# Kernel optimization log

Hardware: AMD Instinct MI355X
Metric: run time of the kernel (lower is better)

## Reference

```python
import jax, jax.numpy as jnp
import numpy as np

ALPHA = 0.05   # propalpha
GDEP = 2       # gcn_depth
DIL = 2        # new_dilation
KSET = (2, 3, 6, 7)

def _dconv(x, w, b, d):
    # Conv2d(c_in, c_out, (1, k), dilation=(1, d), padding='same'), NCHW layout
    k = w.shape[-1]
    tot = d * (k - 1)
    lo = tot // 2
    y = jax.lax.conv_general_dilated(x, w, (1, 1), ((0, 0), (lo, tot - lo)),
                                     rhs_dilation=(1, d),
                                     dimension_numbers=('NCHW', 'OIHW', 'NCHW'))
    return y + b[None, :, None, None]

def _inception(x, ws, bs):
    # 'same' padding keeps seq_len for every branch, so the tail-slice is a no-op
    return jnp.concatenate([_dconv(x, w, b, DIL) for w, b in zip(ws, bs)], axis=1)

def _gcn(Hf, Aoff, W, b, n):
    # PyG GCNConv with unit edge weights (no edge_weight passed) and remaining self-loops:
    # out = D^-1/2 (A_off + I_R)^T D^-1/2 (Hf @ W^T) + b, where only rows < n carry edges.
    XW = Hf @ W.T
    deg = jnp.ones((Hf.shape[0],), Hf.dtype).at[:n].add(jnp.sum(Aoff, axis=0))
    dis = jax.lax.rsqrt(deg)
    out = XW / deg[:, None]                                           # self-loop term
    out = out.at[:n].add(dis[:n, None] * (Aoff.T @ (dis[:n, None] * XW[:n])))
    return out + b[None, :]

def _mixprop(X, A, gws, gbs, mw, mb):
    B, C, n, L = X.shape
    # dense_to_sparse ignores weights here (none passed to GCNConv) -> binary adjacency;
    # add_remaining_self_loops replaces any diagonal entries, so zero the diagonal.
    Aoff = (A != 0).astype(X.dtype) * (1.0 - jnp.eye(n, dtype=X.dtype))
    H = X
    hops = [X]
    for i in range(GDEP):
        Hf = H.reshape(B * L, C * n)   # torch row-major reshape, replicated exactly
        H1 = _gcn(Hf, Aoff, gws[i], gbs[i], n)
        H = ALPHA * X + H1.reshape(B, C, n, L)
        hops.append(H)
    Hc = jnp.concatenate(hops, axis=1)  # (B, (GDEP+1)*C, n, L)
    return jnp.einsum('bixl,oi->boxl', Hc, mw) + mb[None, :, None, None]

def _layernorm(x, w, b, idx, eps=1e-5):
    # F.layer_norm over all of x.shape[1:] with node-indexed affine params
    mu = jnp.mean(x, axis=(1, 2, 3), keepdims=True)
    var = jnp.var(x, axis=(1, 2, 3), keepdims=True)
    xh = (x - mu) * jax.lax.rsqrt(var + eps)
    return xh * w[:, idx, :][None] + b[:, idx, :][None]

def _forward(x, x_skip, A, idx, fws, fbs, gws, gbs, skip_w, skip_b,
             mp1_gw, mp1_gb, mp1_mw, mp1_mb, mp2_gw, mp2_gb, mp2_mw, mp2_mb,
             ln_w, ln_b):
    x_res = x
    xf = jnp.tanh(_inception(x, fws, fbs))
    xg = jax.nn.sigmoid(_inception(x, gws, gbs))
    x = xf * xg  # gated dilated temporal conv (dropout is an eval-mode no-op)
    x_skip = jnp.einsum('bixl,oi->boxl', x, skip_w) + skip_b[None, :, None, None] + x_skip
    x = (_mixprop(x, A, mp1_gw, mp1_gb, mp1_mw, mp1_mb)
         + _mixprop(x.swapaxes(0, 0), A.T, mp2_gw, mp2_gb, mp2_mw, mp2_mb))
    x = x + x_res[..., -x.shape[3]:]
    x = _layernorm(x, ln_w, ln_b, idx)
    return x, x_skip

def setup_inputs():
    key = jax.random.key(0)
    ks = jax.random.split(key, 32)
    B, C, N, L, SKIP = 16, 32, 128, 128, 64
    F = C * N
    co = C // len(KSET)
    d = {}
    d['x'] = jax.random.normal(ks[0], (B, C, N, L), jnp.float32)
    d['x_skip'] = jax.random.normal(ks[1], (B, SKIP, N, L), jnp.float32)
    d['A'] = jax.random.uniform(ks[2], (N, N), jnp.float32)
    d['idx'] = jnp.arange(N, dtype=jnp.int32)
    i = 3
    for pre in ('f', 'g'):
        for k in KSET:
            d[pre + 'w' + str(k)] = jax.random.normal(ks[i], (co, C, 1, k), jnp.float32) * float(1.0 / np.sqrt(C * k))
            d[pre + 'b' + str(k)] = jax.random.uniform(ks[i + 1], (co,), jnp.float32)
            i += 2
    d['skip_w'] = jax.random.normal(ks[i], (SKIP, C), jnp.float32) * float(1.0 / np.sqrt(C)); i += 1
    d['skip_b'] = jax.random.uniform(ks[i], (SKIP,), jnp.float32); i += 1
    for mp in ('mp1', 'mp2'):
        d[mp + '_gw'] = jax.random.normal(ks[i], (GDEP, F, F), jnp.float32) * float(1.0 / np.sqrt(F)); i += 1
        d[mp + '_gb'] = jnp.zeros((GDEP, F), jnp.float32)
        d[mp + '_mw'] = jax.random.normal(ks[i], (C, (GDEP + 1) * C), jnp.float32) * float(1.0 / np.sqrt((GDEP + 1) * C)); i += 1
        d[mp + '_mb'] = jax.random.uniform(ks[i], (C,), jnp.float32); i += 1
    d['ln_w'] = jnp.ones((C, N, L), jnp.float32)
    d['ln_b'] = jnp.zeros((C, N, L), jnp.float32)
    return d

def reference(x, x_skip, A, idx, fw2, fb2, fw3, fb3, fw6, fb6, fw7, fb7,
              gw2, gb2, gw3, gb3, gw6, gb6, gw7, gb7, skip_w, skip_b,
              mp1_gw, mp1_gb, mp1_mw, mp1_mb, mp2_gw, mp2_gb, mp2_mw, mp2_mb,
              ln_w, ln_b):
    return _forward(x, x_skip, A, idx,
                    [fw2, fw3, fw6, fw7], [fb2, fb3, fb6, fb7],
                    [gw2, gw3, gw6, gw7], [gb2, gb3, gb6, gb7],
                    skip_w, skip_b, mp1_gw, mp1_gb, mp1_mw, mp1_mb,
                    mp2_gw, mp2_gb, mp2_mw, mp2_mb, ln_w, ln_b)
```

## Files before the change

kernel.cpp:

```cpp
#include <hip/hip_runtime.h>
#include <stdint.h>

typedef unsigned short u16;
typedef unsigned int   u32;
typedef __attribute__((ext_vector_type(4))) float f32x4;
typedef __attribute__((ext_vector_type(8))) short bf16x8;

__device__ __forceinline__ u16 f2bf(float f) {
    u32 i = __float_as_uint(f);
    u32 r = (i + 0x7fffu + ((i >> 16) & 1u)) >> 16;
    return (u16)r;
}
__device__ __forceinline__ float bf2f(u16 u) {
    return __uint_as_float(((u32)u) << 16);
}
__device__ __forceinline__ u32 cvt2bf(float a, float b) {
    u32 r;
    asm("v_cvt_pk_bf16_f32 %0, %1, %2" : "=v"(r) : "v"(a), "v"(b));
    return r;
}

#define GLOAD16(g, l) __builtin_amdgcn_global_load_lds( \
    (const __attribute__((address_space(1))) void*)(g), \
    (__attribute__((address_space(3))) void*)(l), 16, 0, 0)

#define RAW_BARRIER()  asm volatile("s_barrier" ::: "memory")
#define VMCNT(n)       asm volatile("s_waitcnt vmcnt(" #n ")" ::: "memory")

__global__ void k_prep(const float* __restrict__ A, float* dis1, float* inv1,
                       float* dis2, float* inv2)
{
    int r = threadIdx.x;
    if (r >= 128) return;
    int cc = 0, cr = 0;
    for (int j = 0; j < 128; ++j) {
        if (j == r) continue;
        if (A[(j << 7) + r] != 0.f) cc++;
        if (A[(r << 7) + j] != 0.f) cr++;
    }
    float d1 = 1.f + (float)cc, d2 = 1.f + (float)cr;
    dis1[r] = rsqrtf(d1); inv1[r] = 1.f / d1;
    dis2[r] = rsqrtf(d2); inv2[r] = 1.f / d2;
}

__global__ __launch_bounds__(256)
void k_wcvt2(const float* __restrict__ W0, const float* __restrict__ W1,
             u16* __restrict__ Wb0, u16* __restrict__ Wb1)
{
    int half = blockIdx.x >> 13;
    const float* W = half ? W1 : W0;
    u16* Wb = half ? Wb1 : Wb0;
    size_t e = ((size_t)(blockIdx.x & 8191) * 256 + threadIdx.x) * 8;
    f32x4 a = *(const f32x4*)(W + e);
    f32x4 b = *(const f32x4*)(W + e + 4);
    uint4 r;
    r.x = cvt2bf(a[0], a[1]); r.y = cvt2bf(a[2], a[3]);
    r.z = cvt2bf(b[0], b[1]); r.w = cvt2bf(b[2], b[3]);
    *(uint4*)(Wb + e) = r;
}

__global__ __launch_bounds__(512, 1)
void k_gemm2g(const u16* __restrict__ A0, const u16* __restrict__ A1,
              const u16* __restrict__ B0, const u16* __restrict__ B1,
              const u16* __restrict__ Gres,
              const float* __restrict__ gb0, const float* __restrict__ gb1,
              u16* __restrict__ Ha, u16* __restrict__ Hb,
              float* __restrict__ XW0a, float* __restrict__ XW0b)
{
    __shared__ alignas(16) u16 LDS[65536];
    const int NT = 128;
    const int tid  = threadIdx.x;
    const int lane = tid & 63;
    const int wid  = tid >> 6;
    const int wr = wid >> 2, wc = wid & 3;

    const int bid = blockIdx.x;
    const int swz = (bid & 7) * 32 + (bid >> 3);
    const int z   = swz >> 7;
    const int rem = swz & 127;
    const int bm = (rem >> 4) * 256;
    const int bn = (rem & 15) * 256;

    const u16* Ap = (z ? A1 : A0) + (size_t)bm * 4096;
    const u16* Bp = (z ? B1 : B0) + (size_t)bn * 4096;

    int aoff[8], boff[4];
    #pragma unroll
    for (int i = 0; i < 8; ++i) {
        int row = wr * 128 + i * 16 + (lane & 15);
        int sp  = (lane >> 4) ^ ((row >> 1) & 3);
        aoff[i] = row * 32 + sp * 8;
    }
    #pragma unroll
    for (int j = 0; j < 4; ++j) {
        int row = wc * 64 + j * 16 + (lane & 15);
        int sp  = (lane >> 4) ^ ((row >> 1) & 3);
        boff[j] = row * 32 + sp * 8;
    }

    auto stage = [&](int t) {
        if (t >= NT) return;
        const int k0  = t << 5;
        u16* buf = LDS + ((t & 3) << 14);
        #pragma unroll
        for (int h = 0; h < 2; ++h) {
            const int c  = tid + h * 512;
            const int r  = c >> 2;
            const int sl = (c & 3) ^ ((r >> 1) & 3);
            GLOAD16(Ap + (size_t)r * 4096 + k0 + sl * 8, buf + c * 8);
            GLOAD16(Bp + (size_t)r * 4096 + k0 + sl * 8, buf + 8192 + c * 8);
        }
    };

    f32x4 acc[8][4] = {};

    auto compute = [&](int t) {
        const u16* buf = LDS + ((t & 3) << 14);
        bf16x8 af[8], bf[4];
        #pragma unroll
        for (int j = 0; j < 4; ++j) bf[j] = *(const bf16x8*)(buf + 8192 + boff[j]);
        #pragma unroll
        for (int i = 0; i < 8; ++i) af[i] = *(const bf16x8*)(buf + aoff[i]);
        __builtin_amdgcn_s_setprio(1);
        #pragma unroll
        for (int i = 0; i < 8; ++i)
            #pragma unroll
            for (int j = 0; j < 4; ++j)
                acc[i][j] = __builtin_amdgcn_mfma_f32_16x16x32_bf16(af[i], bf[j], acc[i][j], 0, 0, 0);
        __builtin_amdgcn_s_setprio(0);
    };

    stage(0); stage(1); stage(2);
    for (int t = 0; t < NT - 3; ++t) {
        VMCNT(8);
        RAW_BARRIER();
        stage(t + 3);
        compute(t);
    }
    VMCNT(8);  RAW_BARRIER(); compute(NT - 3);
    VMCNT(4);  RAW_BARRIER(); compute(NT - 2);
    VMCNT(0);  RAW_BARRIER(); compute(NT - 1);

    const int orow = (lane >> 4) * 4, ocol = lane & 15;
    const float* gbv = z ? gb1 : gb0;
    u16* H = z ? Hb : Ha;

    #pragma unroll
    for (int j = 0; j < 4; ++j) {
        const int o = bn + wc * 64 + j * 16 + ocol;
        const float gbo = gbv[o];
        #pragma unroll
        for (int i = 0; i < 8; ++i) {
            const int rbase = bm + wr * 128 + i * 16 + orow;
            #pragma unroll
            for (int v = 0; v < 4; ++v) {
                const size_t e = (size_t)(rbase + v) * 4096 + o;
                float g = bf2f(Gres[e]);
                H[e] = f2bf(__fmaf_rn(0.05f, g, acc[i][j][v] + gbo));
            }
        }
    }
    if (bm == 0 && wr == 0) {
        float* XW0 = z ? XW0b : XW0a;
        #pragma unroll
        for (int i = 0; i < 8; ++i) {
            #pragma unroll
            for (int j = 0; j < 4; ++j) {
                float* cp = XW0 + (size_t)(i * 16 + orow) * 4096 + (bn + wc * 64 + j * 16 + ocol);
                #pragma unroll
                for (int v = 0; v < 4; ++v)
                    cp[(size_t)v * 4096] = acc[i][j][v];
            }
        }
    }
}

__global__ __launch_bounds__(256)
void k_gcnfix(const float* __restrict__ XW0a, const float* __restrict__ XW0b,
              const u16* __restrict__ G, const float* __restrict__ Af,
              const float* __restrict__ dis1, const float* __restrict__ inv1,
              const float* __restrict__ dis2, const float* __restrict__ inv2,
              const float* __restrict__ gb0, const float* __restrict__ gb1,
              u16* __restrict__ Ha, u16* __restrict__ Hb)
{
    const int prob = blockIdx.x >> 9;
    const int rem  = blockIdx.x & 511;
    const int t4 = rem * 256 + threadIdx.x;
    const int r = t4 >> 10, og = (t4 & 1023) << 2;
    const float* XW0 = prob ? XW0b : XW0a;
    const float* dis = prob ? dis2 : dis1;
    const float* inv = prob ? inv2 : inv1;
    const float* gb  = prob ? gb1  : gb0;
    u16* H = prob ? Hb : Ha;

    const size_t e = ((size_t)r << 12) + og;
    f32x4 xw = *(const f32x4*)(XW0 + e);
    f32x4 s = {0.f, 0.f, 0.f, 0.f};
    for (int j = 0; j < 128; ++j) {
        float av = prob ? Af[(r << 7) + j] : Af[(j << 7) + r];
        float wv = ((av != 0.f) && (j != r)) ? dis[j] : 0.f;
        f32x4 xv = *(const f32x4*)(XW0 + ((size_t)j << 12) + og);
        #pragma unroll
        for (int q = 0; q < 4; ++q) s[q] = __fmaf_rn(wv, xv[q], s[q]);
    }
    const float iv = inv[r], dr = dis[r];
    f32x4 gb4 = *(const f32x4*)(gb + og);
    uint2 gv = *(const uint2*)(G + e);
    float g0 = __uint_as_float(gv.x << 16), g1 = __uint_as_float(gv.x & 0xffff0000u);
    float g2 = __uint_as_float(gv.y << 16), g3 = __uint_as_float(gv.y & 0xffff0000u);
    float y0 = __fmaf_rn(0.05f, g0, __fmaf_rn(dr, s[0], xw[0] * iv) + gb4[0]);
    float y1 = __fmaf_rn(0.05f, g1, __fmaf_rn(dr, s[1], xw[1] * iv) + gb4[1]);
    float y2 = __fmaf_rn(0.05f, g2, __fmaf_rn(dr, s[2], xw[2] * iv) + gb4[2]);
    float y3 = __fmaf_rn(0.05f, g3, __fmaf_rn(dr, s[3], xw[3] * iv) + gb4[3]);
    uint2 rr;
    rr.x = cvt2bf(y0, y1);
    rr.y = cvt2bf(y2, y3);
    *(uint2*)(H + e) = rr;
}

__device__ __forceinline__ constexpr int wbase_of(int k) {
    return k == 2 ? 0 : k == 3 ? 520 : k == 6 ? 1296 : 2840;
}
__device__ __forceinline__ constexpr int ob_of(int k) {
    return k == 2 ? 0 : k == 3 ? 8 : k == 6 ? 16 : 24;
}

template<int K_>
__device__ __forceinline__ void conv_phase(const float* __restrict__ xsb,
                                           const float* __restrict__ wfp,
                                           const float* __restrict__ wgp,
                                           float fb, float gb,
                                           u16* __restrict__ Gp)
{
    float accf[8], accg[8];
    #pragma unroll
    for (int i = 0; i < 8; ++i) { accf[i] = fb; accg[i] = gb; }
    for (int c = 0; c < 32; ++c) {
        float xw[24];
        const float* xr = xsb + c * 144;
        #pragma unroll
        for (int q = 0; q < 6; ++q) {
            f32x4 v = *(const f32x4*)(xr + q * 4);
            xw[q * 4 + 0] = v[0]; xw[q * 4 + 1] = v[1];
            xw[q * 4 + 2] = v[2]; xw[q * 4 + 3] = v[3];
        }
        float wfj[K_], wgj[K_];
        const float* wfc = wfp + c * K_;
        const float* wgc = wgp + c * K_;
        #pragma unroll
        for (int j = 0; j < K_; ++j) { wfj[j] = wfc[j]; wgj[j] = wgc[j]; }
        #pragma unroll
        for (int li = 0; li < 8; ++li) {
            #pragma unroll
            for (int j = 0; j < K_; ++j) {
                float xv = xw[li + 8 - (K_ - 1) + 2 * j];
                accf[li] = __fmaf_rn(xv, wfj[j], accf[li]);
                accg[li] = __fmaf_rn(xv, wgj[j], accg[li]);
            }
        }
    }
    u16 o8[8];
    #pragma unroll
    for (int i = 0; i < 8; ++i) {
        float e2 = __expf(2.f * accf[i]);
        float th = 1.f - __fdividef(2.f, e2 + 1.f);
        float sg = __fdividef(1.f, 1.f + __expf(-accg[i]));
        o8[i] = f2bf(th * sg);
    }
    uint4 u;
    u.x = o8[0] | ((u32)o8[1] << 16); u.y = o8[2] | ((u32)o8[3] << 16);
    u.z = o8[4] | ((u32)o8[5] << 16); u.w = o8[6] | ((u32)o8[7] << 16);
    *(uint4*)Gp = u;
}

template<int KA, int KB>
__device__ __forceinline__ void wave_pair(const float* __restrict__ xs,
                                          const float* __restrict__ wfl,
                                          const float* __restrict__ wgl,
                                          const float* __restrict__ fbl,
                                          const float* __restrict__ gbl,
                                          int oo, int lL, int b, int n,
                                          u16* __restrict__ G)
{
    {
        constexpr int BS = wbase_of(KA), ST = 32 * KA + 1, OB = ob_of(KA);
        const int o = OB + oo, l0 = lL * 8;
        conv_phase<KA>(xs + l0, wfl + BS + oo * ST, wgl + BS + oo * ST,
                       fbl[o], gbl[o],
                       G + (((size_t)(b * 32 + o) * 128 + n) * 128 + l0));
    }
    {
        constexpr int BS = wbase_of(KB), ST = 32 * KB + 1, OB = ob_of(KB);
        const int o = OB + oo, l0 = 64 + lL * 8;
        conv_phase<KB>(xs + l0, wfl + BS + oo * ST, wgl + BS + oo * ST,
                       fbl[o], gbl[o],
                       G + (((size_t)(b * 32 + o) * 128 + n) * 128 + l0));
    }
}

__global__ __launch_bounds__(256)
void k_incep(const float* __restrict__ x,
             const float* __restrict__ fw2p, const float* __restrict__ fw3p,
             const float* __restrict__ fw6p, const float* __restrict__ fw7p,
             const float* __restrict__ fb2p, const float* __restrict__ fb3p,
             const float* __restrict__ fb6p, const float* __restrict__ fb7p,
             const float* __restrict__ gw2p, const float* __restrict__ gw3p,
             const float* __restrict__ gw6p, const float* __restrict__ gw7p,
             const float* __restrict__ gb2p, const float* __restrict__ gb3p,
             const float* __restrict__ gb6p, const float* __restrict__ gb7p,
             u16* __restrict__ G)
{
    __shared__ alignas(16) float xs[32 * 144];
    __shared__ float wfl[4640], wgl[4640];
    __shared__ float fbl[32], gbl[32];
    const int tid = threadIdx.x;
    const int b = blockIdx.x >> 7, n = blockIdx.x & 127;

    for (int i = tid; i < 32 * 144; i += 256) xs[i] = 0.f;
    for (int g = tid; g < 4608; g += 256) {
        int rel, k, woff;
        const float *pf, *pg;
        if (g < 512)       { rel = g;        k = 2; woff = 0;    pf = fw2p; pg = gw2p; }
        else if (g < 1280) { rel = g - 512;  k = 3; woff = 520;  pf = fw3p; pg = gw3p; }
        else if (g < 2816) { rel = g - 1280; k = 6; woff = 1296; pf = fw6p; pg = gw6p; }
        else               { rel = g - 2816; k = 7; woff = 2840; pf = fw7p; pg = gw7p; }
        int ck = 32 * k;
        int oo = rel / ck, rem = rel % ck;
        int dst = woff + oo * (ck + 1) + rem;
        wfl[dst] = pf[rel];
        wgl[dst] = pg[rel];
    }
    if (tid < 32) {
        int br = tid >> 3, oo = tid & 7;
        const float* pf = br == 0 ? fb2p : br == 1 ? fb3p : br == 2 ? fb6p : fb7p;
        const float* pg = br == 0 ? gb2p : br == 1 ? gb3p : br == 2 ? gb6p : gb7p;
        fbl[tid] = pf[oo]; gbl[tid] = pg[oo];
    }
    __syncthreads();
    const float* xb = x + (size_t)b * 524288 + n * 128;
    for (int p = 0; p < 4; ++p) {
        int chunk = p * 256 + tid;
        int c = chunk >> 5, l4 = (chunk & 31) * 4;
        *(f32x4*)&xs[c * 144 + 8 + l4] = *(const f32x4*)(xb + (size_t)c * 16384 + l4);
    }
    __syncthreads();

    const int w = tid >> 6, lane = tid & 63;
    const int oo = lane >> 3, lL = lane & 7;
    switch (w) {
        case 0:  wave_pair<2, 7>(xs, wfl, wgl, fbl, gbl, oo, lL, b, n, G); break;
        case 1:  wave_pair<7, 2>(xs, wfl, wgl, fbl, gbl, oo, lL, b, n, G); break;
        case 2:  wave_pair<3, 6>(xs, wfl, wgl, fbl, gbl, oo, lL, b, n, G); break;
        default: wave_pair<6, 3>(xs, wfl, wgl, fbl, gbl, oo, lL, b, n, G); break;
    }
}

__global__ __launch_bounds__(256)
void k_skip(const u16* __restrict__ G, const float* __restrict__ xskip,
            const float* __restrict__ sw, const float* __restrict__ sb,
            float* __restrict__ outp)
{
    __shared__ alignas(16) u16 Gs[4096];
    __shared__ float swl[64 * 33];
    __shared__ float sbl[64];
    const int tid = threadIdx.x;
    const int b = blockIdx.x >> 7, n = blockIdx.x & 127;
    const u16* gb_ = G + (size_t)b * 524288 + n * 128;
    for (int p = 0; p < 2; ++p) {
        int chunk = p * 256 + tid, c = chunk >> 4, l8 = (chunk & 15) * 8;
        *(uint4*)&Gs[c * 128 + l8] = *(const uint4*)(gb_ + (size_t)c * 16384 + l8);
    }
    for (int i = tid; i < 2048; i += 256) swl[(i >> 5) * 33 + (i & 31)] = sw[i];
    if (tid < 64) sbl[tid] = sb[tid];
    __syncthreads();
    const int sg = (tid & 15) * 4, l0 = (tid >> 4) * 8;
    float acc[4][8];
    #pragma unroll
    for (int si = 0; si < 4; ++si) {
        float bv = sbl[sg + si];
        #pragma unroll
        for (int li = 0; li < 8; ++li) acc[si][li] = bv;
    }
    for (int c = 0; c < 32; ++c) {
        uint4 gv = *(const uint4*)&Gs[c * 128 + l0];
        float g[8];
        g[0] = __uint_as_float(gv.x << 16); g[1] = __uint_as_float(gv.x & 0xffff0000u);
        g[2] = __uint_as_float(gv.y << 16); g[3] = __uint_as_float(gv.y & 0xffff0000u);
        g[4] = __uint_as_float(gv.z << 16); g[5] = __uint_as_float(gv.z & 0xffff0000u);
        g[6] = __uint_as_float(gv.w << 16); g[7] = __uint_as_float(gv.w & 0xffff0000u);
        #pragma unroll
        for (int si = 0; si < 4; ++si) {
            float wv = swl[(sg + si) * 33 + c];
            #pragma unroll
            for (int li = 0; li < 8; ++li) acc[si][li] = __fmaf_rn(g[li], wv, acc[si][li]);
        }
    }
    #pragma unroll
    for (int si = 0; si < 4; ++si) {
        size_t e = ((size_t)(b * 64 + sg + si) * 128 + n) * 128 + l0;
        f32x4 x0 = *(const f32x4*)(xskip + e);
        f32x4 x1 = *(const f32x4*)(xskip + e + 4);
        f32x4 r0, r1;
        r0[0] = acc[si][0] + x0[0]; r0[1] = acc[si][1] + x0[1];
        r0[2] = acc[si][2] + x0[2]; r0[3] = acc[si][3] + x0[3];
        r1[0] = acc[si][4] + x1[0]; r1[1] = acc[si][5] + x1[1];
        r1[2] = acc[si][6] + x1[2]; r1[3] = acc[si][7] + x1[3];
        *(f32x4*)(outp + e)     = r0;
        *(f32x4*)(outp + e + 4) = r1;
    }
}

__global__ __launch_bounds__(256)
void k_mix2ln(const u16* __restrict__ G,
              const u16* __restrict__ H1, const u16* __restrict__ H2,
              const u16* __restrict__ H1b, const u16* __restrict__ H2b,
              const float* __restrict__ mw1, const float* __restrict__ mb1,
              const float* __restrict__ mw2, const float* __restrict__ mb2,
              const float* __restrict__ x,
              u16* __restrict__ Y, float* __restrict__ partial)
{
    __shared__ alignas(16) u16 Gs[4096], H1s[4096], H2s[4096], H1bs[4096], H2bs[4096];
    __shared__ float wSg[32 * 33], wS11[32 * 33], wS12[32 * 33], wS21[32 * 33], wS22[32 * 33];
    __shared__ float mbl[32];
    const int tid = threadIdx.x;
    const int b = blockIdx.x >> 7, xn = blockIdx.x & 127;
    size_t base = (size_t)b * 524288 + xn * 128;
    for (int p = 0; p < 2; ++p) {
        int chunk = p * 256 + tid, c = chunk >> 4, l8 = (chunk & 15) * 8;
        size_t src = base + (size_t)c * 16384 + l8;
        *(uint4*)&Gs[c * 128 + l8]   = *(const uint4*)(G + src);
        *(uint4*)&H1s[c * 128 + l8]  = *(const uint4*)(H1 + src);
        *(uint4*)&H2s[c * 128 + l8]  = *(const uint4*)(H2 + src);
        *(uint4*)&H1bs[c * 128 + l8] = *(const uint4*)(H1b + src);
        *(uint4*)&H2bs[c * 128 + l8] = *(const uint4*)(H2b + src);
    }
    for (int i = tid; i < 1024; i += 256) {
        int o = i >> 5, c = i & 31;
        int d = o * 33 + c;
        wSg[d]  = mw1[o * 96 + c] + mw2[o * 96 + c];
        wS11[d] = mw1[o * 96 + 32 + c];
        wS12[d] = mw1[o * 96 + 64 + c];
        wS21[d] = mw2[o * 96 + 32 + c];
        wS22[d] = mw2[o * 96 + 64 + c];
    }
    if (tid < 32) mbl[tid] = mb1[tid] + mb2[tid];
    __syncthreads();
    const int og = (tid & 7) * 4, l0 = (tid >> 3) * 4;
    float acc[4][4];
    #pragma unroll
    for (int oi = 0; oi < 4; ++oi) {
        float bv = mbl[og + oi];
        acc[oi][0] = bv; acc[oi][1] = bv; acc[oi][2] = bv; acc[oi][3] = bv;
    }
    for (int c = 0; c < 32; ++c) {
        uint2 ga = *(const uint2*)&Gs[c * 128 + l0];
        uint2 h1 = *(const uint2*)&H1s[c * 128 + l0];
        uint2 h2 = *(const uint2*)&H2s[c * 128 + l0];
        uint2 j1 = *(const uint2*)&H1bs[c * 128 + l0];
        uint2 j2 = *(const uint2*)&H2bs[c * 128 + l0];
        float gv[4], v1[4], v2[4], u1[4], u2[4];
        gv[0] = __uint_as_float(ga.x << 16); gv[1] = __uint_as_float(ga.x & 0xffff0000u);
        gv[2] = __uint_as_float(ga.y << 16); gv[3] = __uint_as_float(ga.y & 0xffff0000u);
        v1[0] = __uint_as_float(h1.x << 16); v1[1] = __uint_as_float(h1.x & 0xffff0000u);
        v1[2] = __uint_as_float(h1.y << 16); v1[3] = __uint_as_float(h1.y & 0xffff0000u);
        v2[0] = __uint_as_float(h2.x << 16); v2[1] = __uint_as_float(h2.x & 0xffff0000u);
        v2[2] = __uint_as_float(h2.y << 16); v2[3] = __uint_as_float(h2.y & 0xffff0000u);
        u1[0] = __uint_as_float(j1.x << 16); u1[1] = __uint_as_float(j1.x & 0xffff0000u);
        u1[2] = __uint_as_float(j1.y << 16); u1[3] = __uint_as_float(j1.y & 0xffff0000u);
        u2[0] = __uint_as_float(j2.x << 16); u2[1] = __uint_as_float(j2.x & 0xffff0000u);
        u2[2] = __uint_as_float(j2.y << 16); u2[3] = __uint_as_float(j2.y & 0xffff0000u);
        #pragma unroll
        for (int oi = 0; oi < 4; ++oi) {
            int d = (og + oi) * 33 + c;
            float a0 = wSg[d], a1 = wS11[d], a2 = wS12[d], a3 = wS21[d], a4 = wS22[d];
            #pragma unroll
            for (int li = 0; li < 4; ++li)
                acc[oi][li] += gv[li] * a0 + v1[li] * a1 + v2[li] * a2
                             + u1[li] * a3 + u2[li] * a4;
        }
    }
    float s = 0.f, ss = 0.f;
    #pragma unroll
    for (int oi = 0; oi < 4; ++oi) {
        size_t e = ((size_t)(b * 32 + og + oi) * 128 + xn) * 128 + l0;
        f32x4 xv = *(const f32x4*)(x + e);
        float y0 = acc[oi][0] + xv[0];
        float y1 = acc[oi][1] + xv[1];
        float y2 = acc[oi][2] + xv[2];
        float y3 = acc[oi][3] + xv[3];
        s  += y0 + y1 + y2 + y3;
        ss += y0 * y0 + y1 * y1 + y2 * y2 + y3 * y3;
        uint2 rr;
        rr.x = cvt2bf(y0, y1);
        rr.y = cvt2bf(y2, y3);
        *(uint2*)(Y + e) = rr;
    }
    #pragma unroll
    for (int o = 32; o > 0; o >>= 1) {
        s  += __shfl_down(s,  o, 64);
        ss += __shfl_down(ss, o, 64);
    }
    __shared__ float sred[8];
    int w = tid >> 6;
    if ((tid & 63) == 0) { sred[w * 2] = s; sred[w * 2 + 1] = ss; }
    __syncthreads();
    if (tid == 0) {
        partial[blockIdx.x * 2]     = sred[0] + sred[2] + sred[4] + sred[6];
        partial[blockIdx.x * 2 + 1] = sred[1] + sred[3] + sred[5] + sred[7];
    }
}

__global__ __launch_bounds__(256)
void k_lnnorm(const u16* __restrict__ Y,
              const float* __restrict__ partial, const int* __restrict__ idxp,
              const float* __restrict__ lnw, const float* __restrict__ lnb,
              float* __restrict__ outx)
{
    const int tid = threadIdx.x;
    const int b = blockIdx.x >> 7, chunk = blockIdx.x & 127;
    float s = 0.f, ss = 0.f;
    if (tid < 128) {
        s  = partial[(b * 128 + tid) * 2];
        ss = partial[(b * 128 + tid) * 2 + 1];
    }
    #pragma unroll
    for (int o = 32; o > 0; o >>= 1) {
        s  += __shfl_down(s,  o, 64);
        ss += __shfl_down(ss, o, 64);
    }
    __shared__ float sred[4];
    __shared__ float mv[2];
    if ((tid & 63) == 0 && tid < 128) { sred[(tid >> 6) * 2] = s; sred[(tid >> 6) * 2 + 1] = ss; }
    __syncthreads();
    if (tid == 0) {
        float S = sred[0] + sred[2], SS = sred[1] + sred[3];
        float mean = S * (1.f / 524288.f);
        float var = SS * (1.f / 524288.f) - mean * mean;
        mv[0] = mean; mv[1] = rsqrtf(var + 1e-5f);
    }
    __syncthreads();
    const float mean = mv[0], rstd = mv[1];
    #pragma unroll
    for (int q = 0; q < 4; ++q) {
        int ib = chunk * 4096 + q * 1024 + tid * 4;
        size_t e = (size_t)b * 524288 + ib;
        uint2 yv2 = *(const uint2*)(Y + e);
        float y[4];
        y[0] = __uint_as_float(yv2.x << 16); y[1] = __uint_as_float(yv2.x & 0xffff0000u);
        y[2] = __uint_as_float(yv2.y << 16); y[3] = __uint_as_float(yv2.y & 0xffff0000u);
        int c = ib >> 14, xn = (ib >> 7) & 127, l = ib & 127;
        int ix = idxp[xn];
        size_t we = ((size_t)c * 128 + ix) * 128 + l;
        f32x4 wv = *(const f32x4*)(lnw + we);
        f32x4 bv = *(const f32x4*)(lnb + we);
        f32x4 r;
        #pragma unroll
        for (int j = 0; j < 4; ++j)
            r[j] = (y[j] - mean) * rstd * wv[j] + bv[j];
        *(f32x4*)(outx + e) = r;
    }
}

extern "C" void kernel_launch(void* const* d_in, const int* in_sizes, int n_in,
                              void* d_out, int out_size, void* d_ws, size_t ws_size,
                              hipStream_t stream)
{
    (void)in_sizes; (void)n_in; (void)out_size; (void)ws_size;
    const float* x      = (const float*)d_in[0];
    const float* xskip  = (const float*)d_in[1];
    const float* A      = (const float*)d_in[2];
    const int*   idxp   = (const int*)d_in[3];
    const float* fw2p = (const float*)d_in[4];  const float* fb2p = (const float*)d_in[5];
    const float* fw3p = (const float*)d_in[6];  const float* fb3p = (const float*)d_in[7];
    const float* fw6p = (const float*)d_in[8];  const float* fb6p = (const float*)d_in[9];
    const float* fw7p = (const float*)d_in[10]; const float* fb7p = (const float*)d_in[11];
    const float* gw2p = (const float*)d_in[12]; const float* gb2p = (const float*)d_in[13];
    const float* gw3p = (const float*)d_in[14]; const float* gb3p = (const float*)d_in[15];
    const float* gw6p = (const float*)d_in[16]; const float* gb6p = (const float*)d_in[17];
    const float* gw7p = (const float*)d_in[18]; const float* gb7p = (const float*)d_in[19];
    const float* sw   = (const float*)d_in[20]; const float* sb   = (const float*)d_in[21];
    const float* mp1_gw = (const float*)d_in[22]; const float* mp1_gb = (const float*)d_in[23];
    const float* mp1_mw = (const float*)d_in[24]; const float* mp1_mb = (const float*)d_in[25];
    const float* mp2_gw = (const float*)d_in[26]; const float* mp2_gb = (const float*)d_in[27];
    const float* mp2_mw = (const float*)d_in[28]; const float* mp2_mb = (const float*)d_in[29];
    const float* lnw = (const float*)d_in[30]; const float* lnb = (const float*)d_in[31];

    char* wsb = (char*)d_ws;
    float* out_x  = (float*)d_out;
    float* out_sk = out_x + 8388608;

    const size_t MB16 = 16777216, MB33 = 33554432;
    u16*   G    = (u16*)(wsb);
    u16*   H1   = (u16*)(wsb + MB16);
    u16*   H1b  = (u16*)(wsb + 2 * MB16);
    u16*   H2   = (u16*)(wsb + 3 * MB16);
    u16*   H2b  = (u16*)(wsb + 4 * MB16);
    u16*   Wb0  = (u16*)(wsb + 5 * MB16);
    u16*   Wb1  = (u16*)(wsb + 5 * MB16 + MB33);
    u16*   Yb   = (u16*)Wb0;
    float* XW0a = (float*)(wsb + 5 * MB16 + 2 * MB33);
    float* XW0b = (float*)(wsb + 5 * MB16 + 2 * MB33 + 2097152);
    float* part = (float*)(wsb + 5 * MB16 + 2 * MB33 + 4194304);
    float* dd   = (float*)(wsb + 5 * MB16 + 2 * MB33 + 4194304 + 16384);
    float *dis1 = dd, *inv1 = dd + 128, *dis2 = dd + 256, *inv2 = dd + 384;

    k_prep<<<1, 128, 0, stream>>>(A, dis1, inv1, dis2, inv2);
    k_incep<<<2048, 256, 0, stream>>>(x, fw2p, fw3p, fw6p, fw7p, fb2p, fb3p, fb6p, fb7p,
                                      gw2p, gw3p, gw6p, gw7p, gb2p, gb3p, gb6p, gb7p, G);
    k_skip<<<2048, 256, 0, stream>>>(G, xskip, sw, sb, out_sk);

    k_wcvt2<<<16384, 256, 0, stream>>>(mp1_gw, mp2_gw, Wb0, Wb1);
    k_gemm2g<<<256, 512, 0, stream>>>(G, G, Wb0, Wb1, G, mp1_gb, mp2_gb,
                                      H1, H1b, XW0a, XW0b);
    k_gcnfix<<<1024, 256, 0, stream>>>(XW0a, XW0b, G, A, dis1, inv1, dis2, inv2,
                                       mp1_gb, mp2_gb, H1, H1b);
    k_wcvt2<<<16384, 256, 0, stream>>>(mp1_gw + MB16, mp2_gw + MB16, Wb0, Wb1);
    k_gemm2g<<<256, 512, 0, stream>>>(H1, H1b, Wb0, Wb1, G, mp1_gb + 4096, mp2_gb + 4096,
                                      H2, H2b, XW0a, XW0b);
    k_gcnfix<<<1024, 256, 0, stream>>>(XW0a, XW0b, G, A, dis1, inv1, dis2, inv2,
                                       mp1_gb + 4096, mp2_gb + 4096, H2, H2b);
    k_mix2ln<<<2048, 256, 0, stream>>>(G, H1, H2, H1b, H2b, mp1_mw, mp1_mb,
                                       mp2_mw, mp2_mb, x, Yb, part);
    k_lnnorm<<<2048, 256, 0, stream>>>(Yb, part, idxp, lnw, lnb, out_x);
}
```

Baseline: 669.4 us.

## Fuse inception conv and skip conv into one kernel sharing LDS tile

Merges the inception kernel and the skip-conv kernel so the gated conv output is written both to global memory and to shared memory, and the skip 1x1 conv then reads it from LDS instead of re-reading G from global. This removes one kernel launch and a global read of G. The per-wave work is also reorganised: each wave now computes two branches at once over the same input window with interleaved accumulators, where before it handled two branches one after the other on different halves of the sequence. This adds LDS usage and register pressure, which may lower occupancy.

```diff
diff --git a/kernel.cpp b/kernel.cpp
--- a/kernel.cpp
+++ b/kernel.cpp
@@ -225,16 +225,22 @@
     return k == 2 ? 0 : k == 3 ? 8 : k == 6 ? 16 : 24;
 }
 
-template<int K_>
-__device__ __forceinline__ void conv_phase(const float* __restrict__ xsb,
-                                           const float* __restrict__ wfp,
-                                           const float* __restrict__ wgp,
-                                           float fb, float gb,
-                                           u16* __restrict__ Gp)
-{
-    float accf[8], accg[8];
-    #pragma unroll
-    for (int i = 0; i < 8; ++i) { accf[i] = fb; accg[i] = gb; }
+template<int KA, int KB>
+__device__ __forceinline__ void conv_dual(const float* __restrict__ xsb,
+                                          const float* __restrict__ wfA,
+                                          const float* __restrict__ wgA,
+                                          const float* __restrict__ wfB,
+                                          const float* __restrict__ wgB,
+                                          float fbA, float gbA, float fbB, float gbB,
+                                          u16* __restrict__ GpA, u16* __restrict__ GpB,
+                                          u16* __restrict__ GsA, u16* __restrict__ GsB)
+{
+    float afA[8], agA[8], afB[8], agB[8];
+    #pragma unroll
+    for (int i = 0; i < 8; ++i) {
+        afA[i] = fbA; agA[i] = gbA;
+        afB[i] = fbB; agB[i] = gbB;
+    }
     for (int c = 0; c < 32; ++c) {
         float xw[24];
         const float* xr = xsb + c * 144;
@@ -244,75 +250,80 @@
             xw[q * 4 + 0] = v[0]; xw[q * 4 + 1] = v[1];
             xw[q * 4 + 2] = v[2]; xw[q * 4 + 3] = v[3];
         }
-        float wfj[K_], wgj[K_];
-        const float* wfc = wfp + c * K_;
-        const float* wgc = wgp + c * K_;
-        #pragma unroll
-        for (int j = 0; j < K_; ++j) { wfj[j] = wfc[j]; wgj[j] = wgc[j]; }
-        #pragma unroll
-        for (int li = 0; li < 8; ++li) {
-            #pragma unroll
-            for (int j = 0; j < K_; ++j) {
-                float xv = xw[li + 8 - (K_ - 1) + 2 * j];
-                accf[li] = __fmaf_rn(xv, wfj[j], accf[li]);
-                accg[li] = __fmaf_rn(xv, wgj[j], accg[li]);
+        {
+            float wf[KA], wg[KA];
+            const float* pf = wfA + c * KA;
+            const float* pg = wgA + c * KA;
+            #pragma unroll
+            for (int j = 0; j < KA; ++j) { wf[j] = pf[j]; wg[j] = pg[j]; }
+            #pragma unroll
+            for (int li = 0; li < 8; ++li) {
+                #pragma unroll
+                for (int j = 0; j < KA; ++j) {
+                    float xv = xw[li + 8 - (KA - 1) + 2 * j];
+                    afA[li] = __fmaf_rn(xv, wf[j], afA[li]);
+                    agA[li] = __fmaf_rn(xv, wg[j], agA[li]);
+                }
             }
         }
-    }
-    u16 o8[8];
+        {
+            float wf[KB], wg[KB];
+            const float* pf = wfB + c * KB;
+            const float* pg = wgB + c * KB;
+            #pragma unroll
+            for (int j = 0; j < KB; ++j) { wf[j] = pf[j]; wg[j] = pg[j]; }
+            #pragma unroll
+            for (int li = 0; li < 8; ++li) {
+                #pragma unroll
+                for (int j = 0; j < KB; ++j) {
+                    float xv = xw[li + 8 - (KB - 1) + 2 * j];
+                    afB[li] = __fmaf_rn(xv, wf[j], afB[li]);
+                    agB[li] = __fmaf_rn(xv, wg[j], agB[li]);
+                }
+            }
+        }
+    }
+    u16 oA[8], oB[8];
     #pragma unroll
     for (int i = 0; i < 8; ++i) {
-        float e2 = __expf(2.f * accf[i]);
+        float e2 = __expf(2.f * afA[i]);
         float th = 1.f - __fdividef(2.f, e2 + 1.f);
-        float sg = __fdividef(1.f, 1.f + __expf(-accg[i]));
-        o8[i] = f2bf(th * sg);
-    }
-    uint4 u;
-    u.x = o8[0] | ((u32)o8[1] << 16); u.y = o8[2] | ((u32)o8[3] << 16);
-    u.z = o8[4] | ((u32)o8[5] << 16); u.w = o8[6] | ((u32)o8[7] << 16);
-    *(uint4*)Gp = u;
-}
-
-template<int KA, int KB>
-__device__ __forceinline__ void wave_pair(const float* __restrict__ xs,
-                                          const float* __restrict__ wfl,
-                                          const float* __restrict__ wgl,
-                                          const float* __restrict__ fbl,
-                                          const float* __restrict__ gbl,
-                                          int oo, int lL, int b, int n,
-                                          u16* __restrict__ G)
-{
-    {
-        constexpr int BS = wbase_of(KA), ST = 32 * KA + 1, OB = ob_of(KA);
-        const int o = OB + oo, l0 = lL * 8;
-        conv_phase<KA>(xs + l0, wfl + BS + oo * ST, wgl + BS + oo * ST,
-                       fbl[o], gbl[o],
-                       G + (((size_t)(b * 32 + o) * 128 + n) * 128 + l0));
-    }
-    {
-        constexpr int BS = wbase_of(KB), ST = 32 * KB + 1, OB = ob_of(KB);
-        const int o = OB + oo, l0 = 64 + lL * 8;
-        conv_phase<KB>(xs + l0, wfl + BS + oo * ST, wgl + BS + oo * ST,
-                       fbl[o], gbl[o],
-                       G + (((size_t)(b * 32 + o) * 128 + n) * 128 + l0));
-    }
+        float sg = __fdividef(1.f, 1.f + __expf(-agA[i]));
+        oA[i] = f2bf(th * sg);
+        float e2b = __expf(2.f * afB[i]);
+        float thb = 1.f - __fdividef(2.f, e2b + 1.f);
+        float sgb = __fdividef(1.f, 1.f + __expf(-agB[i]));
+        oB[i] = f2bf(thb * sgb);
+    }
+    uint4 uA, uB;
+    uA.x = oA[0] | ((u32)oA[1] << 16); uA.y = oA[2] | ((u32)oA[3] << 16);
+    uA.z = oA[4] | ((u32)oA[5] << 16); uA.w = oA[6] | ((u32)oA[7] << 16);
+    uB.x = oB[0] | ((u32)oB[1] << 16); uB.y = oB[2] | ((u32)oB[3] << 16);
+    uB.z = oB[4] | ((u32)oB[5] << 16); uB.w = oB[6] | ((u32)oB[7] << 16);
+    *(uint4*)GpA = uA; *(uint4*)GpB = uB;
+    *(uint4*)GsA = uA; *(uint4*)GsB = uB;
 }
 
 __global__ __launch_bounds__(256)
-void k_incep(const float* __restrict__ x,
-             const float* __restrict__ fw2p, const float* __restrict__ fw3p,
-             const float* __restrict__ fw6p, const float* __restrict__ fw7p,
-             const float* __restrict__ fb2p, const float* __restrict__ fb3p,
-             const float* __restrict__ fb6p, const float* __restrict__ fb7p,
-             const float* __restrict__ gw2p, const float* __restrict__ gw3p,
-             const float* __restrict__ gw6p, const float* __restrict__ gw7p,
-             const float* __restrict__ gb2p, const float* __restrict__ gb3p,
-             const float* __restrict__ gb6p, const float* __restrict__ gb7p,
-             u16* __restrict__ G)
+void k_incskip(const float* __restrict__ x,
+               const float* __restrict__ fw2p, const float* __restrict__ fw3p,
+               const float* __restrict__ fw6p, const float* __restrict__ fw7p,
+               const float* __restrict__ fb2p, const float* __restrict__ fb3p,
+               const float* __restrict__ fb6p, const float* __restrict__ fb7p,
+               const float* __restrict__ gw2p, const float* __restrict__ gw3p,
+               const float* __restrict__ gw6p, const float* __restrict__ gw7p,
+               const float* __restrict__ gb2p, const float* __restrict__ gb3p,
+               const float* __restrict__ gb6p, const float* __restrict__ gb7p,
+               const float* __restrict__ sw,   const float* __restrict__ sb,
+               const float* __restrict__ xskip,
+               u16* __restrict__ G, float* __restrict__ outp)
 {
     __shared__ alignas(16) float xs[32 * 144];
     __shared__ float wfl[4640], wgl[4640];
     __shared__ float fbl[32], gbl[32];
+    __shared__ alignas(16) u16 Gs[4096];
+    __shared__ float swl[64 * 33];
+    __shared__ float sbl[64];
     const int tid = threadIdx.x;
     const int b = blockIdx.x >> 7, n = blockIdx.x & 127;
 
@@ -330,6 +341,8 @@
         wfl[dst] = pf[rel];
         wgl[dst] = pg[rel];
     }
+    for (int i = tid; i < 2048; i += 256) swl[(i >> 5) * 33 + (i & 31)] = sw[i];
+    if (tid < 64) sbl[tid] = sb[tid];
     if (tid < 32) {
         int br = tid >> 3, oo = tid & 7;
         const float* pf = br == 0 ? fb2p : br == 1 ? fb3p : br == 2 ? fb6p : fb7p;
@@ -345,35 +358,36 @@
     }
     __syncthreads();
 
-    const int w = tid >> 6, lane = tid & 63;
-    const int oo = lane >> 3, lL = lane & 7;
-    switch (w) {
-        case 0:  wave_pair<2, 7>(xs, wfl, wgl, fbl, gbl, oo, lL, b, n, G); break;
-        case 1:  wave_pair<7, 2>(xs, wfl, wgl, fbl, gbl, oo, lL, b, n, G); break;
-        case 2:  wave_pair<3, 6>(xs, wfl, wgl, fbl, gbl, oo, lL, b, n, G); break;
-        default: wave_pair<6, 3>(xs, wfl, wgl, fbl, gbl, oo, lL, b, n, G); break;
-    }
-}
-
-__global__ __launch_bounds__(256)
-void k_skip(const u16* __restrict__ G, const float* __restrict__ xskip,
-            const float* __restrict__ sw, const float* __restrict__ sb,
-            float* __restrict__ outp)
-{
-    __shared__ alignas(16) u16 Gs[4096];
-    __shared__ float swl[64 * 33];
-    __shared__ float sbl[64];
-    const int tid = threadIdx.x;
-    const int b = blockIdx.x >> 7, n = blockIdx.x & 127;
-    const u16* gb_ = G + (size_t)b * 524288 + n * 128;
-    for (int p = 0; p < 2; ++p) {
-        int chunk = p * 256 + tid, c = chunk >> 4, l8 = (chunk & 15) * 8;
-        *(uint4*)&Gs[c * 128 + l8] = *(const uint4*)(gb_ + (size_t)c * 16384 + l8);
-    }
-    for (int i = tid; i < 2048; i += 256) swl[(i >> 5) * 33 + (i & 31)] = sw[i];
-    if (tid < 64) sbl[tid] = sb[tid];
+    {
+        const int w = tid >> 6, lane = tid & 63;
+        const int oo = lane >> 3, lL = lane & 7;
+        const int h  = w & 1;
+        const int l0 = h * 64 + lL * 8;
+        const float* xsb = xs + l0;
+        size_t gbase = ((size_t)b * 32 * 128 + n) * 128 + l0;
+        if (w < 2) {
+            constexpr int KA = 2, KB = 7;
+            const int oA = ob_of(KA) + oo, oB = ob_of(KB) + oo;
+            conv_dual<KA, KB>(xsb,
+                wfl + wbase_of(KA) + oo * (32 * KA + 1), wgl + wbase_of(KA) + oo * (32 * KA + 1),
+                wfl + wbase_of(KB) + oo * (32 * KB + 1), wgl + wbase_of(KB) + oo * (32 * KB + 1),
+                fbl[oA], gbl[oA], fbl[oB], gbl[oB],
+                G + gbase + (size_t)oA * 16384, G + gbase + (size_t)oB * 16384,
+                Gs + oA * 128 + l0, Gs + oB * 128 + l0);
+        } else {
+            constexpr int KA = 3, KB = 6;
+            const int oA = ob_of(KA) + oo, oB = ob_of(KB) + oo;
+            conv_dual<KA, KB>(xsb,
+                wfl + wbase_of(KA) + oo * (32 * KA + 1), wgl + wbase_of(KA) + oo * (32 * KA + 1),
+                wfl + wbase_of(KB) + oo * (32 * KB + 1), wgl + wbase_of(KB) + oo * (32 * KB + 1),
+                fbl[oA], gbl[oA], fbl[oB], gbl[oB],
+                G + gbase + (size_t)oA * 16384, G + gbase + (size_t)oB * 16384,
+                Gs + oA * 128 + l0, Gs + oB * 128 + l0);
+        }
+    }
     __syncthreads();
-    const int sg = (tid & 15) * 4, l0 = (tid >> 4) * 8;
+
+    const int sg = (tid & 15) * 4, l0s = (tid >> 4) * 8;
     float acc[4][8];
     #pragma unroll
     for (int si = 0; si < 4; ++si) {
@@ -382,7 +396,7 @@
         for (int li = 0; li < 8; ++li) acc[si][li] = bv;
     }
     for (int c = 0; c < 32; ++c) {
-        uint4 gv = *(const uint4*)&Gs[c * 128 + l0];
+        uint4 gv = *(const uint4*)&Gs[c * 128 + l0s];
         float g[8];
         g[0] = __uint_as_float(gv.x << 16); g[1] = __uint_as_float(gv.x & 0xffff0000u);
         g[2] = __uint_as_float(gv.y << 16); g[3] = __uint_as_float(gv.y & 0xffff0000u);
@@ -397,7 +411,7 @@
     }
     #pragma unroll
     for (int si = 0; si < 4; ++si) {
-        size_t e = ((size_t)(b * 64 + sg + si) * 128 + n) * 128 + l0;
+        size_t e = ((size_t)(b * 64 + sg + si) * 128 + n) * 128 + l0s;
         f32x4 x0 = *(const f32x4*)(xskip + e);
         f32x4 x1 = *(const f32x4*)(xskip + e + 4);
         f32x4 r0, r1;
@@ -605,9 +619,9 @@
     float *dis1 = dd, *inv1 = dd + 128, *dis2 = dd + 256, *inv2 = dd + 384;
 
     k_prep<<<1, 128, 0, stream>>>(A, dis1, inv1, dis2, inv2);
-    k_incep<<<2048, 256, 0, stream>>>(x, fw2p, fw3p, fw6p, fw7p, fb2p, fb3p, fb6p, fb7p,
-                                      gw2p, gw3p, gw6p, gw7p, gb2p, gb3p, gb6p, gb7p, G);
-    k_skip<<<2048, 256, 0, stream>>>(G, xskip, sw, sb, out_sk);
+    k_incskip<<<2048, 256, 0, stream>>>(x, fw2p, fw3p, fw6p, fw7p, fb2p, fb3p, fb6p, fb7p,
+                                        gw2p, gw3p, gw6p, gw7p, gb2p, gb3p, gb6p, gb7p,
+                                        sw, sb, xskip, G, out_sk);
 
     k_wcvt2<<<16384, 256, 0, stream>>>(mp1_gw, mp2_gw, Wb0, Wb1);
     k_gemm2g<<<256, 512, 0, stream>>>(G, G, Wb0, Wb1, G, mp1_gb, mp2_gb,
```

Result: faster. 649.3 us (-3.0%).
